# Kernel optimization log

Measured on AMD Instinct MI355X. Metric: run time of the kernel, lower is better.

## Reference

```python
import jax, jax.numpy as jnp
import numpy as np

EPS = 1e-18
MARGIN = 0.2  # hp.margin (cancels: positive/positive == 1)
BIAS = 1.0    # hp.bias


def setup_inputs() -> dict:
    key = jax.random.key(0)
    k1, k2, k3, k4 = jax.random.split(key, 4)
    B, T, D = 32, 256, 256  # T == D required by the broadcast in Ecos_sim
    return {
        "pre_VF": jax.random.normal(k1, (B, T, D), dtype=jnp.float32),
        "pre_AF": jax.random.normal(k2, (B, T, D), dtype=jnp.float32),
        "back_VF": jax.random.normal(k3, (B, T, D), dtype=jnp.float32),
        "back_AF": jax.random.normal(k4, (B, T, D), dtype=jnp.float32),
    }


def _direction_loss(V, A):
    """For each anchor i: log(1 + sum_{j != i} exp(sim(V_i, A_j))).

    sim(V_i, A_j)[t, s] = (V_i @ A_j.T)[t, s] / (||V_i||_F * colnorm(A_j)[s])
    (faithful to Ecos_sim: scalar Frobenius norm for V, per-column norm for A,
    broadcast along the last axis; positive/positive == 1 exactly, so the
    positive term and margin cancel.)
    """
    B = V.shape[0]
    # upper[i,j,t,s] = <V[i,t,:], A[j,s,:]>
    upper = jnp.einsum("itd,jsd->ijts", V, A)
    v_norm = jnp.sqrt(jnp.sum(V ** 2, axis=(1, 2)) + EPS)      # [B]
    a_norm = jnp.sqrt(jnp.sum(A ** 2, axis=1) + EPS)           # [B, D]
    sim = upper / (v_norm[:, None, None, None] * a_norm[None, :, None, :])
    e_sim = jnp.exp(sim)                                        # [B,B,T,T]
    idx = jnp.arange(B)
    down = e_sim.sum(axis=1) - e_sim[idx, idx]                  # exclude j == i
    rows = jnp.log(1.0 + down)                                  # [B,T,T]
    return rows.reshape(-1, rows.shape[-1])                     # cat along dim 0


def reference(pre_VF, pre_AF, back_VF, back_AF):
    sim_back_V = _direction_loss(back_VF, back_AF)
    sim_back_A = _direction_loss(back_AF, back_VF)
    return -(1.0 / BIAS) * (sim_back_V + sim_back_A)
```

## Files before the change

kernel.cpp:

```cpp
#include <hip/hip_runtime.h>
#include <cstdint>

#define R_TOT 8192
#define KD    256
#define SLOT  ((size_t)R_TOT * KD)
#define IVN_OFF  0
#define ICN_OFF  256
#define CSQ_OFF  (ICN_OFF + 65536)
#define MATS_OFF (CSQ_OFF + 524288)

typedef float f32x4 __attribute__((ext_vector_type(4)));
typedef int   i32x4 __attribute__((ext_vector_type(4)));
typedef int   i32x8 __attribute__((ext_vector_type(8)));

__device__ __forceinline__ void glds16(const void* g, void* l){
  __builtin_amdgcn_global_load_lds((const __attribute__((address_space(1))) uint32_t*)g,
                                   (__attribute__((address_space(3))) uint32_t*)l, 16, 0, 0);
}

__global__ void cast_ns_k(const float* __restrict__ V, const float* __restrict__ A,
                          unsigned char* __restrict__ mats, float* __restrict__ csq){
  const int tc = blockIdx.x, j = blockIdx.y, ten = blockIdx.z;
  const int tid = threadIdx.x;
  const int g    = tid & 31;
  const int tsub = tid >> 5;
  const int c    = g >> 1;
  const int half = g & 1;
  const float* X = (ten ? A : V) + (size_t)j * 65536;
  unsigned char* M = mats + (size_t)ten * SLOT + (size_t)j * 65536;
  float cs[8];
  #pragma unroll
  for (int e = 0; e < 8; ++e) cs[e] = 0.f;
  #pragma unroll
  for (int tt = 0; tt < 4; ++tt){
    const int t = tc * 32 + tt * 8 + tsub;
    const float4 p0 = *(const float4*)(X + t * 256 + g * 8);
    const float4 p1 = *(const float4*)(X + t * 256 + g * 8 + 4);
    cs[0] += p0.x * p0.x; cs[1] += p0.y * p0.y; cs[2] += p0.z * p0.z; cs[3] += p0.w * p0.w;
    cs[4] += p1.x * p1.x; cs[5] += p1.y * p1.y; cs[6] += p1.z * p1.z; cs[7] += p1.w * p1.w;
    int d0 = __builtin_amdgcn_cvt_pk_fp8_f32(p0.x, p0.y, 0, false);
    d0     = __builtin_amdgcn_cvt_pk_fp8_f32(p0.z, p0.w, d0, true);
    int d1 = __builtin_amdgcn_cvt_pk_fp8_f32(p1.x, p1.y, 0, false);
    d1     = __builtin_amdgcn_cvt_pk_fp8_f32(p1.z, p1.w, d1, true);
    int2 o; o.x = d0; o.y = d1;
    *(int2*)(M + (size_t)t * 256 + (((c ^ (t & 15)) << 4) | (half << 3))) = o;
  }
  __shared__ float red[8][256];
  #pragma unroll
  for (int e = 0; e < 8; ++e) red[tsub][g * 8 + e] = cs[e];
  __syncthreads();
  float s = 0.f;
  #pragma unroll
  for (int gg = 0; gg < 8; ++gg) s += red[gg][tid];
  csq[(size_t)((tc * 2 + ten) * 32 + j) * 256 + tid] = s;
}

__global__ void nreduce_k(const float* __restrict__ csq, float* __restrict__ ivn,
                          float* __restrict__ icn){
  const int j = blockIdx.x, ten = blockIdx.y, s = threadIdx.x;
  float c = 0.f;
  #pragma unroll
  for (int tc = 0; tc < 8; ++tc)
    c += csq[(size_t)((tc * 2 + ten) * 32 + j) * 256 + s];
  icn[ten * 8192 + j * 256 + s] = rsqrtf(c + 1e-18f);
  __shared__ float red[256];
  red[s] = c; __syncthreads();
  for (int off = 128; off > 0; off >>= 1){
    if (s < off) red[s] += red[s + off];
    __syncthreads();
  }
  if (s == 0) ivn[ten * 32 + j] = rsqrtf(red[0] + 1e-18f);
}

__global__ __launch_bounds__(256, 2) void gemm_both_k(const unsigned char* __restrict__ mats,
                                                      const float* __restrict__ ivn,
                                                      const float* __restrict__ icn,
                                                      float* __restrict__ out){
  __shared__ __align__(16) char smem[81920];
  const int tid  = threadIdx.x;
  const int lane = tid & 63;
  const int w    = tid >> 6;
  const int dir  = w >> 1;
  const int half = w & 1;
  const int lm   = lane & 15;
  const int kh   = lane >> 4;
  const int s0   = blockIdx.x * 32;
  const int rb   = blockIdx.y;
  const int r0   = rb * 128;
  const int ib   = rb >> 1;

  const unsigned char* rowmat = mats + (size_t)dir * SLOT;
  const unsigned char* colmat = mats + (size_t)(1 - dir) * SLOT;
  const float sivn = ivn[dir * 32 + ib] * 1.44269504088896340736f;

  char* wbase = smem + w * 16384;
  float* cscw = (float*)(smem + 65536) + w * 1024;
  const int lo16 = lane * 16;
  const unsigned char* colbase = colmat + (size_t)s0 * 256;

  auto issue = [&](int x){
    const int j = x + (x >= ib ? 1 : 0);
    const unsigned char* src = colbase + (size_t)j * 65536;
    char* dst = wbase + ((x & 1) << 13);
    #pragma unroll
    for (int c = 0; c < 8; ++c)
      glds16(src + c * 1024 + lo16, dst + c * 1024 + lo16);
  };

  issue(0);

  {
    const int col = lane & 31;
    const float* ib2 = icn + (size_t)(1 - dir) * 8192 + s0 + col;
    #pragma unroll
    for (int jx = 0; jx < 16; ++jx){
      const int j = jx * 2 + (lane >> 5);
      cscw[j * 32 + col] = sivn * ib2[j * 256];
    }
  }

  i32x8 afr[4][2];
  #pragma unroll
  for (int mi = 0; mi < 4; ++mi){
    const unsigned char* rp = rowmat + (size_t)(r0 + half * 64 + mi * 16 + lm) * 256;
    #pragma unroll
    for (int t = 0; t < 2; ++t){
      i32x4 lo = *(const i32x4*)(rp + ((((t << 3) | (kh << 1) | 0) ^ lm) << 4));
      i32x4 hi = *(const i32x4*)(rp + ((((t << 3) | (kh << 1) | 1) ^ lm) << 4));
      afr[mi][t] = i32x8{lo.x, lo.y, lo.z, lo.w, hi.x, hi.y, hi.z, hi.w};
    }
  }
  #pragma unroll
  for (int mi = 0; mi < 4; ++mi)
    #pragma unroll
    for (int t = 0; t < 2; ++t)
      asm volatile("" : "+v"(afr[mi][t]));

  int ad[2][2][2];
  #pragma unroll
  for (int nj = 0; nj < 2; ++nj)
    #pragma unroll
    for (int t = 0; t < 2; ++t)
      #pragma unroll
      for (int u = 0; u < 2; ++u)
        ad[nj][t][u] = (nj * 16 + lm) * 256 + ((((t << 3) | (kh << 1) | u) ^ lm) << 4);

  f32x4 acc[4][2];
  #pragma unroll
  for (int mi = 0; mi < 4; ++mi)
    #pragma unroll
    for (int nj = 0; nj < 2; ++nj)
      acc[mi][nj] = f32x4{0.f, 0.f, 0.f, 0.f};
  const f32x4 fz = {0.f, 0.f, 0.f, 0.f};

  asm volatile("s_waitcnt vmcnt(0) lgkmcnt(0)" ::: "memory");

  #pragma unroll 1
  for (int jj = 0; jj < 31; ++jj){
    const int j = jj + (jj >= ib ? 1 : 0);

    if (jj < 30){
      issue(jj + 1);
      asm volatile("s_waitcnt vmcnt(8)" ::: "memory");
    } else {
      asm volatile("s_waitcnt vmcnt(0)" ::: "memory");
    }

    const char* rbuf = wbase + ((jj & 1) << 13);
    i32x8 b[2][2];
    #pragma unroll
    for (int nj = 0; nj < 2; ++nj)
      #pragma unroll
      for (int t = 0; t < 2; ++t){
        i32x4 lo = *(const i32x4*)(rbuf + ad[nj][t][0]);
        i32x4 hi = *(const i32x4*)(rbuf + ad[nj][t][1]);
        b[t][nj] = i32x8{lo.x, lo.y, lo.z, lo.w, hi.x, hi.y, hi.z, hi.w};
      }
    const float csc0 = cscw[j * 32 + lm];
    const float csc1 = cscw[j * 32 + 16 + lm];

    f32x4 S[4][2];
    #pragma unroll
    for (int mi = 0; mi < 4; ++mi){
      S[mi][0] = __builtin_amdgcn_mfma_scale_f32_16x16x128_f8f6f4(afr[mi][0], b[0][0], fz, 0, 0, 0, 127, 0, 127);
      S[mi][1] = __builtin_amdgcn_mfma_scale_f32_16x16x128_f8f6f4(afr[mi][0], b[0][1], fz, 0, 0, 0, 127, 0, 127);
    }
    #pragma unroll
    for (int mi = 0; mi < 4; ++mi){
      S[mi][0] = __builtin_amdgcn_mfma_scale_f32_16x16x128_f8f6f4(afr[mi][1], b[1][0], S[mi][0], 0, 0, 0, 127, 0, 127);
      S[mi][1] = __builtin_amdgcn_mfma_scale_f32_16x16x128_f8f6f4(afr[mi][1], b[1][1], S[mi][1], 0, 0, 0, 127, 0, 127);
    }

    #pragma unroll
    for (int mi = 0; mi < 4; ++mi){
      const f32x4 t0 = S[mi][0] * csc0;
      const f32x4 t1 = S[mi][1] * csc1;
      f32x4 e0, e1;
      #pragma unroll
      for (int r = 0; r < 4; ++r){ e0[r] = __builtin_amdgcn_exp2f(t0[r]); e1[r] = __builtin_amdgcn_exp2f(t1[r]); }
      acc[mi][0] += e0;
      acc[mi][1] += e1;
    }
  }

  __syncthreads();
  float* ebuf = (float*)smem;
  #pragma unroll
  for (int mi = 0; mi < 4; ++mi){
    #pragma unroll
    for (int nj = 0; nj < 2; ++nj){
      const int n = nj * 16 + lm;
      #pragma unroll
      for (int r = 0; r < 4; ++r){
        const int m = half * 64 + mi * 16 + (kh << 2) + r;
        ebuf[(dir * 128 + m) * 36 + n] = __logf(1.f + acc[mi][nj][r]);
      }
    }
  }
  __syncthreads();
  #pragma unroll
  for (int p = 0; p < 4; ++p){
    const int i   = tid + p * 256;
    const int row = i >> 3;
    const int c4  = i & 7;
    const f32x4 e0 = *(const f32x4*)(&ebuf[row * 36 + c4 * 4]);
    const f32x4 e1 = *(const f32x4*)(&ebuf[(128 + row) * 36 + c4 * 4]);
    f32x4 o;
    #pragma unroll
    for (int e = 0; e < 4; ++e) o[e] = -(e0[e] + e1[e]);
    *(f32x4*)(&out[(size_t)(r0 + row) * 256 + s0 + c4 * 4]) = o;
  }
}

extern "C" void kernel_launch(void* const* d_in, const int* in_sizes, int n_in,
                              void* d_out, int out_size, void* d_ws, size_t ws_size,
                              hipStream_t stream){
  const float* V = (const float*)d_in[2];
  const float* A = (const float*)d_in[3];
  float* out = (float*)d_out;
  float* ivn = (float*)((char*)d_ws + IVN_OFF);
  float* icn = (float*)((char*)d_ws + ICN_OFF);
  float* csq = (float*)((char*)d_ws + CSQ_OFF);
  unsigned char* mats = (unsigned char*)((char*)d_ws + MATS_OFF);

  cast_ns_k<<<dim3(8, 32, 2), 256, 0, stream>>>(V, A, mats, csq);
  nreduce_k<<<dim3(32, 2), 256, 0, stream>>>(csq, ivn, icn);
  gemm_both_k<<<dim3(8, 64), 256, 0, stream>>>(mats, ivn, icn, out);
}
```

Baseline: 120.3 us.

## Share column tiles across four waves per direction with 4-stage LDS ring

```diff
diff --git a/kernel.cpp b/kernel.cpp
--- a/kernel.cpp
+++ b/kernel.cpp
@@ -72,49 +72,50 @@
   if (s == 0) ivn[ten * 32 + j] = rsqrtf(red[0] + 1e-18f);
 }
 
-__global__ __launch_bounds__(256, 2) void gemm_both_k(const unsigned char* __restrict__ mats,
+__global__ __launch_bounds__(512, 2) void gemm_both_k(const unsigned char* __restrict__ mats,
                                                       const float* __restrict__ ivn,
                                                       const float* __restrict__ icn,
                                                       float* __restrict__ out){
-  __shared__ __align__(16) char smem[81920];
+  __shared__ __align__(16) char smem[73728];
   const int tid  = threadIdx.x;
   const int lane = tid & 63;
   const int w    = tid >> 6;
-  const int dir  = w >> 1;
-  const int half = w & 1;
+  const int dir  = w >> 2;
+  const int q    = w & 3;
   const int lm   = lane & 15;
   const int kh   = lane >> 4;
   const int s0   = blockIdx.x * 32;
   const int rb   = blockIdx.y;
-  const int r0   = rb * 128;
-  const int ib   = rb >> 1;
+  const int r0   = rb * 256;
+  const int ib   = rb;
 
   const unsigned char* rowmat = mats + (size_t)dir * SLOT;
   const unsigned char* colmat = mats + (size_t)(1 - dir) * SLOT;
   const float sivn = ivn[dir * 32 + ib] * 1.44269504088896340736f;
 
-  char* wbase = smem + w * 16384;
-  float* cscw = (float*)(smem + 65536) + w * 1024;
+  char*  dbase = smem + dir * 32768;
+  float* cscw  = (float*)(smem + 65536) + dir * 1024;
+  const unsigned char* colbase = colmat + (size_t)s0 * 256;
   const int lo16 = lane * 16;
-  const unsigned char* colbase = colmat + (size_t)s0 * 256;
 
   auto issue = [&](int x){
     const int j = x + (x >= ib ? 1 : 0);
-    const unsigned char* src = colbase + (size_t)j * 65536;
-    char* dst = wbase + ((x & 1) << 13);
-    #pragma unroll
-    for (int c = 0; c < 8; ++c)
-      glds16(src + c * 1024 + lo16, dst + c * 1024 + lo16);
+    const unsigned char* src = colbase + (size_t)j * 65536 + q * 2048;
+    char* dst = dbase + ((x & 3) << 13) + q * 2048;
+    glds16(src + lo16,        dst + lo16);
+    glds16(src + 1024 + lo16, dst + 1024 + lo16);
   };
 
   issue(0);
+  issue(1);
 
   {
     const int col = lane & 31;
+    const int jh  = lane >> 5;
     const float* ib2 = icn + (size_t)(1 - dir) * 8192 + s0 + col;
     #pragma unroll
-    for (int jx = 0; jx < 16; ++jx){
-      const int j = jx * 2 + (lane >> 5);
+    for (int jx = 0; jx < 4; ++jx){
+      const int j = q * 8 + jx * 2 + jh;
       cscw[j * 32 + col] = sivn * ib2[j * 256];
     }
   }
@@ -122,7 +123,7 @@
   i32x8 afr[4][2];
   #pragma unroll
   for (int mi = 0; mi < 4; ++mi){
-    const unsigned char* rp = rowmat + (size_t)(r0 + half * 64 + mi * 16 + lm) * 256;
+    const unsigned char* rp = rowmat + (size_t)(r0 + q * 64 + mi * 16 + lm) * 256;
     #pragma unroll
     for (int t = 0; t < 2; ++t){
       i32x4 lo = *(const i32x4*)(rp + ((((t << 3) | (kh << 1) | 0) ^ lm) << 4));
@@ -154,19 +155,16 @@
   const f32x4 fz = {0.f, 0.f, 0.f, 0.f};
 
   asm volatile("s_waitcnt vmcnt(0) lgkmcnt(0)" ::: "memory");
+  __builtin_amdgcn_s_barrier();
+  __builtin_amdgcn_sched_barrier(0);
 
   #pragma unroll 1
-  for (int jj = 0; jj < 31; ++jj){
-    const int j = jj + (jj >= ib ? 1 : 0);
-
-    if (jj < 30){
-      issue(jj + 1);
-      asm volatile("s_waitcnt vmcnt(8)" ::: "memory");
-    } else {
-      asm volatile("s_waitcnt vmcnt(0)" ::: "memory");
-    }
-
-    const char* rbuf = wbase + ((jj & 1) << 13);
+  for (int x = 0; x < 31; ++x){
+    const int j = x + (x >= ib ? 1 : 0);
+
+    if (x <= 28) issue(x + 2);
+
+    const char* rbuf = dbase + ((x & 3) << 13);
     i32x8 b[2][2];
     #pragma unroll
     for (int nj = 0; nj < 2; ++nj)
@@ -201,6 +199,13 @@
       acc[mi][0] += e0;
       acc[mi][1] += e1;
     }
+
+    if (x <= 28)      asm volatile("s_waitcnt vmcnt(2)" ::: "memory");
+    else if (x == 29) asm volatile("s_waitcnt vmcnt(0)" ::: "memory");
+    if (x < 30){
+      __builtin_amdgcn_s_barrier();
+      __builtin_amdgcn_sched_barrier(0);
+    }
   }
 
   __syncthreads();
@@ -212,19 +217,19 @@
       const int n = nj * 16 + lm;
       #pragma unroll
       for (int r = 0; r < 4; ++r){
-        const int m = half * 64 + mi * 16 + (kh << 2) + r;
-        ebuf[(dir * 128 + m) * 36 + n] = __logf(1.f + acc[mi][nj][r]);
+        const int m = q * 64 + mi * 16 + (kh << 2) + r;
+        ebuf[(dir * 256 + m) * 36 + n] = __logf(1.f + acc[mi][nj][r]);
       }
     }
   }
   __syncthreads();
   #pragma unroll
   for (int p = 0; p < 4; ++p){
-    const int i   = tid + p * 256;
+    const int i   = tid + p * 512;
     const int row = i >> 3;
     const int c4  = i & 7;
     const f32x4 e0 = *(const f32x4*)(&ebuf[row * 36 + c4 * 4]);
-    const f32x4 e1 = *(const f32x4*)(&ebuf[(128 + row) * 36 + c4 * 4]);
+    const f32x4 e1 = *(const f32x4*)(&ebuf[(256 + row) * 36 + c4 * 4]);
     f32x4 o;
     #pragma unroll
     for (int e = 0; e < 4; ++e) o[e] = -(e0[e] + e1[e]);
@@ -245,5 +250,5 @@
 
   cast_ns_k<<<dim3(8, 32, 2), 256, 0, stream>>>(V, A, mats, csq);
   nreduce_k<<<dim3(32, 2), 256, 0, stream>>>(csq, ivn, icn);
-  gemm_both_k<<<dim3(8, 64), 256, 0, stream>>>(mats, ivn, icn, out);
-}
+  gemm_both_k<<<dim3(8, 32), 512, 0, stream>>>(mats, ivn, icn, out);
+}
```

New measurement: 119.2 us. Within noise of the previous version (-0.9%).
